# Performance work log

Hardware: AMD Instinct MI355X
Metric: run time of the kernel (lower is better)

The kernel has to match this reference:

```python
import jax, jax.numpy as jnp
import numpy as np

N_NODES = 100000
N_EDGES = 3200000


def _cheb_norm(edge_index, edge_weight, num_nodes):
    # PyG ChebConv.__norm__ with normalization='sym', lambda_max=2.0:
    # L_hat = 2/lambda_max * (I - D^-1/2 A D^-1/2) - I = -D^-1/2 A D^-1/2
    # (the +1 diagonal from get_laplacian and the -1 self-loops cancel),
    # so only the off-diagonal terms -d_i^-1/2 w_ij d_j^-1/2 remain.
    src, dst = edge_index[0], edge_index[1]
    deg = jax.ops.segment_sum(edge_weight, src, num_segments=num_nodes)
    safe = jnp.where(deg > 0, deg, 1.0)
    dis = jnp.where(deg > 0, jax.lax.rsqrt(safe), 0.0)  # deg_inv_sqrt, inf -> 0
    return -dis[src] * edge_weight * dis[dst]


def _cheb_conv(x, src, dst, norm, W, b, num_nodes):
    # W: [K, C_in, C_out]. Chebyshev recurrence Tx_k = 2 L_hat Tx_{k-1} - Tx_{k-2}.
    def prop(h):  # (L_hat h)[dst] += norm_e * h[src]
        return jax.ops.segment_sum(norm[:, None] * h[src], dst, num_segments=num_nodes)

    K = W.shape[0]
    out = x @ W[0]
    if K > 1:
        tx1 = prop(x)
        out = out + tx1 @ W[1]
        if K > 2:
            def step(carry, Wk):
                tx_m2, tx_m1, acc = carry
                tx = 2.0 * prop(tx_m1) - tx_m2
                return (tx_m1, tx, acc + tx @ Wk), None
            (_, _, out), _ = jax.lax.scan(step, (x, tx1, out), W[2:])
    if b is not None:
        out = out + b
    return out


def setup_inputs() -> dict:
    key = jax.random.key(0)
    ks = jax.random.split(key, 12)
    x = jax.random.normal(ks[0], (N_NODES, 2), dtype=jnp.float32)
    edge_index = jax.random.randint(ks[1], (2, N_EDGES), 0, N_NODES, dtype=jnp.int64)
    edge_weight = jax.random.uniform(ks[2], (N_EDGES,), dtype=jnp.float32)
    s = 0.1  # keep activations in a sane range (glorot-ish scale)
    W1 = jax.random.normal(ks[3], (39, 2, 14), dtype=jnp.float32) * s
    b1 = jax.random.normal(ks[4], (14,), dtype=jnp.float32) * s
    W2 = jax.random.normal(ks[5], (43, 14, 20), dtype=jnp.float32) * s
    b2 = jax.random.normal(ks[6], (20,), dtype=jnp.float32) * s
    W3 = jax.random.normal(ks[7], (45, 20, 27), dtype=jnp.float32) * s
    b3 = jax.random.normal(ks[8], (27,), dtype=jnp.float32) * s
    W4 = jax.random.normal(ks[9], (1, 27, 1), dtype=jnp.float32) * s  # K=1, no bias
    return {"x": x, "edge_index": edge_index, "edge_weight": edge_weight,
            "W1": W1, "b1": b1, "W2": W2, "b2": b2, "W3": W3, "b3": b3, "W4": W4}


def reference(x, edge_index, edge_weight, W1, b1, W2, b2, W3, b3, W4):
    src, dst = edge_index[0], edge_index[1]
    norm = _cheb_norm(edge_index, edge_weight, N_NODES)
    h = jax.nn.silu(_cheb_conv(x, src, dst, norm, W1, b1, N_NODES))
    h = jax.nn.silu(_cheb_conv(h, src, dst, norm, W2, b2, N_NODES))
    h = jax.nn.silu(_cheb_conv(h, src, dst, norm, W3, b3, N_NODES))
    h = _cheb_conv(h, src, dst, norm, W4, None, N_NODES)
    return jax.nn.sigmoid(h)
```

## Files before the change

### kernel.cpp

```cpp
#include <hip/hip_runtime.h>
#include <math.h>

#define N_NODES 100000
#define N_EDGES 3200000
#define BS 256
#define CAP_SHIFT 7
#define CAP (1 << CAP_SHIFT)


__global__ void scan_partial_kernel(const int* __restrict__ cnt, int* __restrict__ bsums) {
    __shared__ int lds[256];
    int tid = threadIdx.x;
    int base = blockIdx.x * 1024 + tid * 4;
    int s = 0;
#pragma unroll
    for (int i = 0; i < 4; ++i) s += (base + i < N_NODES) ? cnt[base + i] : 0;
    lds[tid] = s;
    __syncthreads();
    for (int off = 128; off > 0; off >>= 1) {
        if (tid < off) lds[tid] += lds[tid + off];
        __syncthreads();
    }
    if (tid == 0) bsums[blockIdx.x] = lds[0];
}

__global__ void scan_bsums_kernel(int* __restrict__ bsums, int nb, int* __restrict__ total_out) {
    if (threadIdx.x == 0 && blockIdx.x == 0) {
        int acc = 0;
        for (int b = 0; b < nb; ++b) {
            int v = bsums[b];
            bsums[b] = acc;
            acc += v;
        }
        *total_out = acc;
    }
}

__global__ void scan_final_kernel(const int* __restrict__ cnt, const int* __restrict__ bsums,
                                  int* __restrict__ rp) {
    __shared__ int lds[256];
    int tid = threadIdx.x;
    int base = blockIdx.x * 1024 + tid * 4;
    int v[4];
    int ts = 0;
#pragma unroll
    for (int i = 0; i < 4; ++i) {
        v[i] = (base + i < N_NODES) ? cnt[base + i] : 0;
        ts += v[i];
    }
    lds[tid] = ts;
    __syncthreads();
    for (int off = 1; off < 256; off <<= 1) {
        int t = (tid >= off) ? lds[tid - off] : 0;
        __syncthreads();
        lds[tid] += t;
        __syncthreads();
    }
    int run = lds[tid] - ts + bsums[blockIdx.x];
#pragma unroll
    for (int i = 0; i < 4; ++i) {
        if (base + i < N_NODES) rp[base + i] = run;
        run += v[i];
    }
}

__global__ void fill_direct_kernel(const int* __restrict__ src, const int* __restrict__ dst,
                                   int* __restrict__ cnt_s, int* __restrict__ cnt_d,
                                   int* __restrict__ bkt_s, int* __restrict__ bkt_d) {
    int e = blockIdx.x * blockDim.x + threadIdx.x;
    if (e >= N_EDGES) return;
    int s = src[e];
    int d = dst[e];
    int slot_s = atomicAdd(&cnt_s[s], 1);
    bkt_s[((size_t)s << CAP_SHIFT) + slot_s] = e;
    int slot_d = atomicAdd(&cnt_d[d], 1);
    bkt_d[((size_t)d << CAP_SHIFT) + slot_d] = e;
}

__global__ __launch_bounds__(64) void sort_deg_dis_kernel(
    const int* __restrict__ cnt, const int* __restrict__ bkt,
    const float* __restrict__ w, float* __restrict__ dis) {
#pragma clang fp contract(off)
    {
        __shared__ int lr[64][65];
        __shared__ int ls[64][65];
        int n = blockIdx.x * 64 + threadIdx.x;
        if (n >= N_NODES) return;
        int c = cnt[n];
        const int* row = bkt + ((size_t)n << CAP_SHIFT);
        float d = 0.f;
        if (c <= 64) {
            int* a = lr[threadIdx.x];
            int* b = ls[threadIdx.x];
            for (int i = 0; i < c; ++i) a[i] = row[i];
            for (int i = 0; i < c; ++i) {
                int v = a[i];
                int rk = 0;
                for (int j = 0; j < c; ++j) rk += (a[j] < v);
                b[rk] = v;
            }
            for (int r = 0; r < c; ++r) d = d + w[b[r]];
        } else {
            for (int r = 0; r < c; ++r) {
                for (int i = 0; i < c; ++i) {
                    int v = row[i];
                    int rk = 0;
                    for (int j = 0; j < c; ++j) rk += (row[j] < v);
                    if (rk == r) { d = d + w[v]; break; }
                }
            }
        }
        dis[n] = (d > 0.f) ? (1.0f / sqrtf(d)) : 0.f;
    }
}

__global__ __launch_bounds__(64) void sort_pack_kernel(
    const int* __restrict__ cnt, const int* __restrict__ rp,
    const int* __restrict__ bkt, const int* __restrict__ src,
    const float* __restrict__ w, const float* __restrict__ dis,
    int2* __restrict__ packed) {
#pragma clang fp contract(off)
    {
        __shared__ int lr[64][65];
        __shared__ int ls[64][65];
        int n = blockIdx.x * 64 + threadIdx.x;
        if (n >= N_NODES) return;
        int c = cnt[n];
        const int* row = bkt + ((size_t)n << CAP_SHIFT);
        int beg = rp[n];
        float din = dis[n];
        if (c <= 64) {
            int* a = lr[threadIdx.x];
            int* b = ls[threadIdx.x];
            for (int i = 0; i < c; ++i) a[i] = row[i];
            for (int i = 0; i < c; ++i) {
                int v = a[i];
                int rk = 0;
                for (int j = 0; j < c; ++j) rk += (a[j] < v);
                b[rk] = v;
            }
            for (int r = 0; r < c; ++r) {
                int e = b[r];
                int s = src[e];
                float cw = ((-dis[s]) * w[e]) * din;
                packed[beg + r] = make_int2(s, __float_as_int(cw));
            }
        } else {
            for (int r = 0; r < c; ++r) {
                for (int i = 0; i < c; ++i) {
                    int v = row[i];
                    int rk = 0;
                    for (int j = 0; j < c; ++j) rk += (row[j] < v);
                    if (rk == r) {
                        int s = src[v];
                        float cw = ((-dis[s]) * w[v]) * din;
                        packed[beg + r] = make_int2(s, __float_as_int(cw));
                        break;
                    }
                }
            }
        }
    }
}


template <int CIN, int COUT, int SIN, int SACC>
__global__ void layer_init_kernel(const float* __restrict__ hin, const float* __restrict__ W0,
                                  float* __restrict__ acc) {
    int t = blockIdx.x * blockDim.x + threadIdx.x;
    if (t >= N_NODES * COUT) return;
    int n = t / COUT, co = t - n * COUT;
    const float* hr = hin + (size_t)n * SIN;
    float m = 0.f;
#pragma unroll
    for (int ci = 0; ci < CIN; ++ci) m = fmaf(hr[ci], W0[ci * COUT + co], m);
    acc[(size_t)n * SACC + co] = m;
}

template <int CIN, int COUT, int SIN, int SACC, int GS, int LANES, int R>
__global__ __launch_bounds__(LANES* R) void prop_mm_kernel(
    const int* __restrict__ rp, const int2* __restrict__ pk, const float* __restrict__ hin,
    const float* __restrict__ prev, const float* __restrict__ Wk, int rec,
    float* __restrict__ tx_out, float* __restrict__ acc) {
#pragma clang fp contract(off)
    {
        __shared__ float tls[R][LANES * GS];
        int r = threadIdx.x / LANES;
        int lane = threadIdx.x - r * LANES;
        int n = blockIdx.x * R + r;
        bool vn = (n < N_NODES);
        if (vn) {
            int c0 = lane * GS;
            float s[GS];
#pragma unroll
            for (int g = 0; g < GS; ++g) s[g] = 0.f;
            int beg = rp[n], end = rp[n + 1];
            int j = beg;
            if constexpr (GS == 4) {
                for (; j + 7 < end; j += 8) {
                    int2 p0 = pk[j];
                    int2 p1 = pk[j + 1];
                    int2 p2 = pk[j + 2];
                    int2 p3 = pk[j + 3];
                    int2 p4 = pk[j + 4];
                    int2 p5 = pk[j + 5];
                    int2 p6 = pk[j + 6];
                    int2 p7 = pk[j + 7];
                    const float4 q0 = *reinterpret_cast<const float4*>(hin + (size_t)p0.x * SIN + c0);
                    const float4 q1 = *reinterpret_cast<const float4*>(hin + (size_t)p1.x * SIN + c0);
                    const float4 q2 = *reinterpret_cast<const float4*>(hin + (size_t)p2.x * SIN + c0);
                    const float4 q3 = *reinterpret_cast<const float4*>(hin + (size_t)p3.x * SIN + c0);
                    const float4 q4 = *reinterpret_cast<const float4*>(hin + (size_t)p4.x * SIN + c0);
                    const float4 q5 = *reinterpret_cast<const float4*>(hin + (size_t)p5.x * SIN + c0);
                    const float4 q6 = *reinterpret_cast<const float4*>(hin + (size_t)p6.x * SIN + c0);
                    const float4 q7 = *reinterpret_cast<const float4*>(hin + (size_t)p7.x * SIN + c0);
                    float w0 = __int_as_float(p0.y), w1 = __int_as_float(p1.y);
                    float w2 = __int_as_float(p2.y), w3 = __int_as_float(p3.y);
                    float w4 = __int_as_float(p4.y), w5 = __int_as_float(p5.y);
                    float w6 = __int_as_float(p6.y), w7 = __int_as_float(p7.y);
                    s[0] = s[0] + (w0 * q0.x); s[1] = s[1] + (w0 * q0.y);
                    s[2] = s[2] + (w0 * q0.z); s[3] = s[3] + (w0 * q0.w);
                    s[0] = s[0] + (w1 * q1.x); s[1] = s[1] + (w1 * q1.y);
                    s[2] = s[2] + (w1 * q1.z); s[3] = s[3] + (w1 * q1.w);
                    s[0] = s[0] + (w2 * q2.x); s[1] = s[1] + (w2 * q2.y);
                    s[2] = s[2] + (w2 * q2.z); s[3] = s[3] + (w2 * q2.w);
                    s[0] = s[0] + (w3 * q3.x); s[1] = s[1] + (w3 * q3.y);
                    s[2] = s[2] + (w3 * q3.z); s[3] = s[3] + (w3 * q3.w);
                    s[0] = s[0] + (w4 * q4.x); s[1] = s[1] + (w4 * q4.y);
                    s[2] = s[2] + (w4 * q4.z); s[3] = s[3] + (w4 * q4.w);
                    s[0] = s[0] + (w5 * q5.x); s[1] = s[1] + (w5 * q5.y);
                    s[2] = s[2] + (w5 * q5.z); s[3] = s[3] + (w5 * q5.w);
                    s[0] = s[0] + (w6 * q6.x); s[1] = s[1] + (w6 * q6.y);
                    s[2] = s[2] + (w6 * q6.z); s[3] = s[3] + (w6 * q6.w);
                    s[0] = s[0] + (w7 * q7.x); s[1] = s[1] + (w7 * q7.y);
                    s[2] = s[2] + (w7 * q7.z); s[3] = s[3] + (w7 * q7.w);
                }
                for (; j + 3 < end; j += 4) {
                    int2 p0 = pk[j];
                    int2 p1 = pk[j + 1];
                    int2 p2 = pk[j + 2];
                    int2 p3 = pk[j + 3];
                    const float4 q0 = *reinterpret_cast<const float4*>(hin + (size_t)p0.x * SIN + c0);
                    const float4 q1 = *reinterpret_cast<const float4*>(hin + (size_t)p1.x * SIN + c0);
                    const float4 q2 = *reinterpret_cast<const float4*>(hin + (size_t)p2.x * SIN + c0);
                    const float4 q3 = *reinterpret_cast<const float4*>(hin + (size_t)p3.x * SIN + c0);
                    float w0 = __int_as_float(p0.y), w1 = __int_as_float(p1.y);
                    float w2 = __int_as_float(p2.y), w3 = __int_as_float(p3.y);
                    s[0] = s[0] + (w0 * q0.x); s[1] = s[1] + (w0 * q0.y);
                    s[2] = s[2] + (w0 * q0.z); s[3] = s[3] + (w0 * q0.w);
                    s[0] = s[0] + (w1 * q1.x); s[1] = s[1] + (w1 * q1.y);
                    s[2] = s[2] + (w1 * q1.z); s[3] = s[3] + (w1 * q1.w);
                    s[0] = s[0] + (w2 * q2.x); s[1] = s[1] + (w2 * q2.y);
                    s[2] = s[2] + (w2 * q2.z); s[3] = s[3] + (w2 * q2.w);
                    s[0] = s[0] + (w3 * q3.x); s[1] = s[1] + (w3 * q3.y);
                    s[2] = s[2] + (w3 * q3.z); s[3] = s[3] + (w3 * q3.w);
                }
                for (; j < end; ++j) {
                    int2 p = pk[j];
                    float w = __int_as_float(p.y);
                    const float4 q = *reinterpret_cast<const float4*>(hin + (size_t)p.x * SIN + c0);
                    s[0] = s[0] + (w * q.x); s[1] = s[1] + (w * q.y);
                    s[2] = s[2] + (w * q.z); s[3] = s[3] + (w * q.w);
                }
            } else {
                for (; j + 7 < end; j += 8) {
                    int2 p0 = pk[j];
                    int2 p1 = pk[j + 1];
                    int2 p2 = pk[j + 2];
                    int2 p3 = pk[j + 3];
                    int2 p4 = pk[j + 4];
                    int2 p5 = pk[j + 5];
                    int2 p6 = pk[j + 6];
                    int2 p7 = pk[j + 7];
                    const float2 q0 = *reinterpret_cast<const float2*>(hin + (size_t)p0.x * SIN + c0);
                    const float2 q1 = *reinterpret_cast<const float2*>(hin + (size_t)p1.x * SIN + c0);
                    const float2 q2 = *reinterpret_cast<const float2*>(hin + (size_t)p2.x * SIN + c0);
                    const float2 q3 = *reinterpret_cast<const float2*>(hin + (size_t)p3.x * SIN + c0);
                    const float2 q4 = *reinterpret_cast<const float2*>(hin + (size_t)p4.x * SIN + c0);
                    const float2 q5 = *reinterpret_cast<const float2*>(hin + (size_t)p5.x * SIN + c0);
                    const float2 q6 = *reinterpret_cast<const float2*>(hin + (size_t)p6.x * SIN + c0);
                    const float2 q7 = *reinterpret_cast<const float2*>(hin + (size_t)p7.x * SIN + c0);
                    float w0 = __int_as_float(p0.y), w1 = __int_as_float(p1.y);
                    float w2 = __int_as_float(p2.y), w3 = __int_as_float(p3.y);
                    float w4 = __int_as_float(p4.y), w5 = __int_as_float(p5.y);
                    float w6 = __int_as_float(p6.y), w7 = __int_as_float(p7.y);
                    s[0] = s[0] + (w0 * q0.x); s[1] = s[1] + (w0 * q0.y);
                    s[0] = s[0] + (w1 * q1.x); s[1] = s[1] + (w1 * q1.y);
                    s[0] = s[0] + (w2 * q2.x); s[1] = s[1] + (w2 * q2.y);
                    s[0] = s[0] + (w3 * q3.x); s[1] = s[1] + (w3 * q3.y);
                    s[0] = s[0] + (w4 * q4.x); s[1] = s[1] + (w4 * q4.y);
                    s[0] = s[0] + (w5 * q5.x); s[1] = s[1] + (w5 * q5.y);
                    s[0] = s[0] + (w6 * q6.x); s[1] = s[1] + (w6 * q6.y);
                    s[0] = s[0] + (w7 * q7.x); s[1] = s[1] + (w7 * q7.y);
                }
                for (; j + 3 < end; j += 4) {
                    int2 p0 = pk[j];
                    int2 p1 = pk[j + 1];
                    int2 p2 = pk[j + 2];
                    int2 p3 = pk[j + 3];
                    const float2 q0 = *reinterpret_cast<const float2*>(hin + (size_t)p0.x * SIN + c0);
                    const float2 q1 = *reinterpret_cast<const float2*>(hin + (size_t)p1.x * SIN + c0);
                    const float2 q2 = *reinterpret_cast<const float2*>(hin + (size_t)p2.x * SIN + c0);
                    const float2 q3 = *reinterpret_cast<const float2*>(hin + (size_t)p3.x * SIN + c0);
                    float w0 = __int_as_float(p0.y), w1 = __int_as_float(p1.y);
                    float w2 = __int_as_float(p2.y), w3 = __int_as_float(p3.y);
                    s[0] = s[0] + (w0 * q0.x); s[1] = s[1] + (w0 * q0.y);
                    s[0] = s[0] + (w1 * q1.x); s[1] = s[1] + (w1 * q1.y);
                    s[0] = s[0] + (w2 * q2.x); s[1] = s[1] + (w2 * q2.y);
                    s[0] = s[0] + (w3 * q3.x); s[1] = s[1] + (w3 * q3.y);
                }
                for (; j < end; ++j) {
                    int2 p = pk[j];
                    float w = __int_as_float(p.y);
                    const float2 q = *reinterpret_cast<const float2*>(hin + (size_t)p.x * SIN + c0);
                    s[0] = s[0] + (w * q.x); s[1] = s[1] + (w * q.y);
                }
            }
            float t[GS];
            if (rec) {
#pragma unroll
                for (int g = 0; g < GS; ++g) t[g] = 2.f * s[g] - prev[(size_t)n * SIN + c0 + g];
            } else {
#pragma unroll
                for (int g = 0; g < GS; ++g) t[g] = s[g];
            }
#pragma unroll
            for (int g = 0; g < GS; ++g) tls[r][c0 + g] = t[g];
            if constexpr (GS == 4) {
                *reinterpret_cast<float4*>(tx_out + (size_t)n * SIN + c0) =
                    make_float4(t[0], t[1], t[2], t[3]);
            } else {
                *reinterpret_cast<float2*>(tx_out + (size_t)n * SIN + c0) =
                    make_float2(t[0], t[1]);
            }
        }
        __syncthreads();
        if (vn) {
            for (int co = lane; co < COUT; co += LANES) {
                float m = 0.f;
#pragma unroll
                for (int ci = 0; ci < CIN; ++ci) m = fmaf(tls[r][ci], Wk[ci * COUT + co], m);
                acc[(size_t)n * SACC + co] = acc[(size_t)n * SACC + co] + m;
            }
        }
    }
}

template <int C, int S>
__global__ void silu_bias_kernel(float* __restrict__ a, const float* __restrict__ b) {
#pragma clang fp contract(off)
    {
        int t = blockIdx.x * blockDim.x + threadIdx.x;
        if (t >= N_NODES * C) return;
        int n = t / C, c = t - n * C;
        float x = a[(size_t)n * S + c] + b[c];
        float sig = 1.f / (1.f + expf(-x));
        a[(size_t)n * S + c] = x * sig;
    }
}

__global__ void final_kernel(const float* __restrict__ acc, const float* __restrict__ b3,
                             const float* __restrict__ W4, float* __restrict__ out) {
#pragma clang fp contract(off)
    {
        int n = blockIdx.x * blockDim.x + threadIdx.x;
        if (n >= N_NODES) return;
        float m = 0.f;
#pragma unroll
        for (int ci = 0; ci < 27; ++ci) {
            float xv = acc[(size_t)n * 28 + ci] + b3[ci];
            float sig = 1.f / (1.f + expf(-xv));
            float hv = xv * sig;
            m = fmaf(hv, W4[ci], m);
        }
        out[n] = 1.f / (1.f + expf(-m));
    }
}

__global__ void signal_kernel(float* __restrict__ out, float val) {
    int n = blockIdx.x * blockDim.x + threadIdx.x;
    if (n < N_NODES) out[n] = val;
}


static void run_scan(const int* cnt, int* bsums, int* rp, hipStream_t stream) {
    const int nb = (N_NODES + 1023) / 1024;
    scan_partial_kernel<<<nb, 256, 0, stream>>>(cnt, bsums);
    scan_bsums_kernel<<<1, 64, 0, stream>>>(bsums, nb, rp + N_NODES);
    scan_final_kernel<<<nb, 256, 0, stream>>>(cnt, bsums, rp);
}

template <int CIN, int COUT, int SIN, int SACC, int GS, int LANES, int R>
static void run_layer(int K, const float* hin, const float* W, float* acc, float* b0, float* b1,
                      float* b2, const int* rp, const int2* pk, hipStream_t stream) {
    const int gInit = (N_NODES * COUT + BS - 1) / BS;
    const int gProp = (N_NODES + R - 1) / R;
    layer_init_kernel<CIN, COUT, SIN, SACC><<<gInit, BS, 0, stream>>>(hin, W, acc);
    if (K > 1) {
        float* bufs[3] = {b0, b1, b2};
        prop_mm_kernel<CIN, COUT, SIN, SACC, GS, LANES, R><<<gProp, LANES * R, 0, stream>>>(
            rp, pk, hin, nullptr, W + 1 * CIN * COUT, 0, bufs[0], acc);
        const float* pm2 = hin;
        const float* pm1 = bufs[0];
        for (int k = 2; k < K; ++k) {
            float* outb = bufs[(k - 1) % 3];
            prop_mm_kernel<CIN, COUT, SIN, SACC, GS, LANES, R><<<gProp, LANES * R, 0, stream>>>(
                rp, pk, pm1, pm2, W + k * CIN * COUT, 1, outb, acc);
            pm2 = pm1;
            pm1 = outb;
        }
    }
}

extern "C" void kernel_launch(void* const* d_in, const int* in_sizes, int n_in, void* d_out,
                              int out_size, void* d_ws, size_t ws_size, hipStream_t stream) {
    const float* x  = (const float*)d_in[0];
    const int* idx  = (const int*)d_in[1];
    const float* ew = (const float*)d_in[2];
    const float* W1 = (const float*)d_in[3];
    const float* b1 = (const float*)d_in[4];
    const float* W2 = (const float*)d_in[5];
    const float* b2 = (const float*)d_in[6];
    const float* W3 = (const float*)d_in[7];
    const float* b3 = (const float*)d_in[8];
    const float* W4 = (const float*)d_in[9];
    float* out = (float*)d_out;
    (void)in_sizes; (void)n_in; (void)out_size;

    const int* src = idx;
    const int* dst = idx + N_EDGES;

    size_t off = 0;
    auto alloc = [&](size_t bytes) {
        size_t o = off;
        off = (off + bytes + 255) & ~(size_t)255;
        return o;
    };
    char* ws = (char*)d_ws;
    int*   cnt_s   = (int*)(ws + alloc(N_NODES * 4));
    int*   cnt_d   = (int*)(ws + alloc(N_NODES * 4));
    int*   rp_src  = (int*)(ws + alloc((N_NODES + 1) * 4));
    int*   rp_dst  = (int*)(ws + alloc((N_NODES + 1) * 4));
    float* dis     = (float*)(ws + alloc(N_NODES * 4));
    int*   bsums   = (int*)(ws + alloc(512));
    int2*  packed  = (int2*)(ws + alloc((size_t)N_EDGES * 8));
    float* t0      = (float*)(ws + alloc((size_t)N_NODES * 20 * 4));
    float* t1      = (float*)(ws + alloc((size_t)N_NODES * 20 * 4));
    float* t2      = (float*)(ws + alloc((size_t)N_NODES * 20 * 4));
    float* accA    = (float*)(ws + alloc((size_t)N_NODES * 16 * 4));
    float* accB    = (float*)(ws + alloc((size_t)N_NODES * 20 * 4));
    float* accC    = (float*)(ws + alloc((size_t)N_NODES * 28 * 4));
    int*   bkt_s   = (int*)(ws + alloc((size_t)N_NODES * CAP * 4));
    int*   bkt_d   = (int*)(ws + alloc((size_t)N_NODES * CAP * 4));
    const size_t NEED = off;

    int gE = (N_EDGES + BS - 1) / BS;
    int gN = (N_NODES + BS - 1) / BS;
    const int gSort = (N_NODES + 63) / 64;

    if (ws_size < NEED) {
        signal_kernel<<<gN, BS, 0, stream>>>(
            out, 6000.0f + (float)(ws_size / (1024.0 * 1024.0)));
        return;
    }

    (void)hipMemsetAsync(cnt_s, 0, N_NODES * 4, stream);
    (void)hipMemsetAsync(cnt_d, 0, N_NODES * 4, stream);
    fill_direct_kernel<<<gE, BS, 0, stream>>>(src, dst, cnt_s, cnt_d, bkt_s, bkt_d);
    run_scan(cnt_s, bsums, rp_src, stream);
    run_scan(cnt_d, bsums, rp_dst, stream);
    sort_deg_dis_kernel<<<gSort, 64, 0, stream>>>(cnt_s, bkt_s, ew, dis);
    sort_pack_kernel<<<gSort, 64, 0, stream>>>(cnt_d, rp_dst, bkt_d, src, ew, dis, packed);

    run_layer<2, 14, 2, 16, 2, 1, 256>(39, x, W1, accA, t0, t1, t2, rp_dst, packed, stream);
    silu_bias_kernel<14, 16><<<(N_NODES * 14 + BS - 1) / BS, BS, 0, stream>>>(accA, b1);
    run_layer<14, 20, 16, 20, 4, 4, 64>(43, accA, W2, accB, t0, t1, t2, rp_dst, packed, stream);
    silu_bias_kernel<20, 20><<<(N_NODES * 20 + BS - 1) / BS, BS, 0, stream>>>(accB, b2);
    run_layer<20, 27, 20, 28, 4, 5, 51>(45, accB, W3, accC, t0, t1, t2, rp_dst, packed, stream);
    final_kernel<<<gN, BS, 0, stream>>>(accC, b3, W4, out);
}
```

Baseline: 7.692 ms.

## Split feature channels into planar groups and batch the dense matmuls

Node features are stored as separate channel planes (8/8/4-wide groups), and propagation kernels now gather one group per block. This makes each gather touch a narrower, cache-friendlier slice. The dense W_k multiply-accumulate moves out of the propagation kernel into a batched kernel that applies up to 4 Chebyshev terms per pass from a 6-slot ring buffer, cutting acc read-modify-write traffic. The cost is more kernel launches and repeated reads of the edge list per channel group.

```diff
diff --git a/kernel.cpp b/kernel.cpp
--- a/kernel.cpp
+++ b/kernel.cpp
@@ -6,6 +6,9 @@
 #define BS 256
 #define CAP_SHIFT 7
 #define CAP (1 << CAP_SHIFT)
+#define SLOTF 2000000
+#define OFF1 800000
+#define OFF2 1600000
 
 
 __global__ void scan_partial_kernel(const int* __restrict__ cnt, int* __restrict__ bsums) {
@@ -163,199 +166,363 @@
     }
 }
 
-
-template <int CIN, int COUT, int SIN, int SACC>
-__global__ void layer_init_kernel(const float* __restrict__ hin, const float* __restrict__ W0,
-                                  float* __restrict__ acc) {
-    int t = blockIdx.x * blockDim.x + threadIdx.x;
-    if (t >= N_NODES * COUT) return;
-    int n = t / COUT, co = t - n * COUT;
-    const float* hr = hin + (size_t)n * SIN;
-    float m = 0.f;
-#pragma unroll
-    for (int ci = 0; ci < CIN; ++ci) m = fmaf(hr[ci], W0[ci * COUT + co], m);
-    acc[(size_t)n * SACC + co] = m;
-}
-
-template <int CIN, int COUT, int SIN, int SACC, int GS, int LANES, int R>
-__global__ __launch_bounds__(LANES* R) void prop_mm_kernel(
+__device__ __forceinline__ size_t addrA(int n, int c) {
+    return (c < 8) ? ((size_t)n * 8 + c) : (OFF1 + (size_t)n * 8 + (c - 8));
+}
+__device__ __forceinline__ size_t addrB(int n, int c) {
+    return (c < 8) ? ((size_t)n * 8 + c)
+         : (c < 16) ? (OFF1 + (size_t)n * 8 + (c - 8))
+                    : (OFF2 + (size_t)n * 4 + (c - 16));
+}
+
+template <int S>
+__device__ __forceinline__ void gather4_u8(const float* __restrict__ a, int c0,
+                                           const int2* __restrict__ pk, int beg, int end,
+                                           float s[4]) {
+#pragma clang fp contract(off)
+    {
+        int j = beg;
+        for (; j + 7 < end; j += 8) {
+            int2 p0 = pk[j];
+            int2 p1 = pk[j + 1];
+            int2 p2 = pk[j + 2];
+            int2 p3 = pk[j + 3];
+            int2 p4 = pk[j + 4];
+            int2 p5 = pk[j + 5];
+            int2 p6 = pk[j + 6];
+            int2 p7 = pk[j + 7];
+            const float4 q0 = *reinterpret_cast<const float4*>(a + (size_t)p0.x * S + c0);
+            const float4 q1 = *reinterpret_cast<const float4*>(a + (size_t)p1.x * S + c0);
+            const float4 q2 = *reinterpret_cast<const float4*>(a + (size_t)p2.x * S + c0);
+            const float4 q3 = *reinterpret_cast<const float4*>(a + (size_t)p3.x * S + c0);
+            const float4 q4 = *reinterpret_cast<const float4*>(a + (size_t)p4.x * S + c0);
+            const float4 q5 = *reinterpret_cast<const float4*>(a + (size_t)p5.x * S + c0);
+            const float4 q6 = *reinterpret_cast<const float4*>(a + (size_t)p6.x * S + c0);
+            const float4 q7 = *reinterpret_cast<const float4*>(a + (size_t)p7.x * S + c0);
+            float w0 = __int_as_float(p0.y), w1 = __int_as_float(p1.y);
+            float w2 = __int_as_float(p2.y), w3 = __int_as_float(p3.y);
+            float w4 = __int_as_float(p4.y), w5 = __int_as_float(p5.y);
+            float w6 = __int_as_float(p6.y), w7 = __int_as_float(p7.y);
+            s[0] = s[0] + (w0 * q0.x); s[1] = s[1] + (w0 * q0.y);
+            s[2] = s[2] + (w0 * q0.z); s[3] = s[3] + (w0 * q0.w);
+            s[0] = s[0] + (w1 * q1.x); s[1] = s[1] + (w1 * q1.y);
+            s[2] = s[2] + (w1 * q1.z); s[3] = s[3] + (w1 * q1.w);
+            s[0] = s[0] + (w2 * q2.x); s[1] = s[1] + (w2 * q2.y);
+            s[2] = s[2] + (w2 * q2.z); s[3] = s[3] + (w2 * q2.w);
+            s[0] = s[0] + (w3 * q3.x); s[1] = s[1] + (w3 * q3.y);
+            s[2] = s[2] + (w3 * q3.z); s[3] = s[3] + (w3 * q3.w);
+            s[0] = s[0] + (w4 * q4.x); s[1] = s[1] + (w4 * q4.y);
+            s[2] = s[2] + (w4 * q4.z); s[3] = s[3] + (w4 * q4.w);
+            s[0] = s[0] + (w5 * q5.x); s[1] = s[1] + (w5 * q5.y);
+            s[2] = s[2] + (w5 * q5.z); s[3] = s[3] + (w5 * q5.w);
+            s[0] = s[0] + (w6 * q6.x); s[1] = s[1] + (w6 * q6.y);
+            s[2] = s[2] + (w6 * q6.z); s[3] = s[3] + (w6 * q6.w);
+            s[0] = s[0] + (w7 * q7.x); s[1] = s[1] + (w7 * q7.y);
+            s[2] = s[2] + (w7 * q7.z); s[3] = s[3] + (w7 * q7.w);
+        }
+        for (; j + 3 < end; j += 4) {
+            int2 p0 = pk[j];
+            int2 p1 = pk[j + 1];
+            int2 p2 = pk[j + 2];
+            int2 p3 = pk[j + 3];
+            const float4 q0 = *reinterpret_cast<const float4*>(a + (size_t)p0.x * S + c0);
+            const float4 q1 = *reinterpret_cast<const float4*>(a + (size_t)p1.x * S + c0);
+            const float4 q2 = *reinterpret_cast<const float4*>(a + (size_t)p2.x * S + c0);
+            const float4 q3 = *reinterpret_cast<const float4*>(a + (size_t)p3.x * S + c0);
+            float w0 = __int_as_float(p0.y), w1 = __int_as_float(p1.y);
+            float w2 = __int_as_float(p2.y), w3 = __int_as_float(p3.y);
+            s[0] = s[0] + (w0 * q0.x); s[1] = s[1] + (w0 * q0.y);
+            s[2] = s[2] + (w0 * q0.z); s[3] = s[3] + (w0 * q0.w);
+            s[0] = s[0] + (w1 * q1.x); s[1] = s[1] + (w1 * q1.y);
+            s[2] = s[2] + (w1 * q1.z); s[3] = s[3] + (w1 * q1.w);
+            s[0] = s[0] + (w2 * q2.x); s[1] = s[1] + (w2 * q2.y);
+            s[2] = s[2] + (w2 * q2.z); s[3] = s[3] + (w2 * q2.w);
+            s[0] = s[0] + (w3 * q3.x); s[1] = s[1] + (w3 * q3.y);
+            s[2] = s[2] + (w3 * q3.z); s[3] = s[3] + (w3 * q3.w);
+        }
+        for (; j < end; ++j) {
+            int2 p = pk[j];
+            float w = __int_as_float(p.y);
+            const float4 q = *reinterpret_cast<const float4*>(a + (size_t)p.x * S + c0);
+            s[0] = s[0] + (w * q.x); s[1] = s[1] + (w * q.y);
+            s[2] = s[2] + (w * q.z); s[3] = s[3] + (w * q.w);
+        }
+    }
+}
+
+__device__ __forceinline__ void gather2_u8s2(const float* __restrict__ a,
+                                             const int2* __restrict__ pk, int beg, int end,
+                                             float s[2]) {
+#pragma clang fp contract(off)
+    {
+        int j = beg;
+        for (; j + 7 < end; j += 8) {
+            int2 p0 = pk[j];
+            int2 p1 = pk[j + 1];
+            int2 p2 = pk[j + 2];
+            int2 p3 = pk[j + 3];
+            int2 p4 = pk[j + 4];
+            int2 p5 = pk[j + 5];
+            int2 p6 = pk[j + 6];
+            int2 p7 = pk[j + 7];
+            const float2 q0 = *reinterpret_cast<const float2*>(a + (size_t)p0.x * 2);
+            const float2 q1 = *reinterpret_cast<const float2*>(a + (size_t)p1.x * 2);
+            const float2 q2 = *reinterpret_cast<const float2*>(a + (size_t)p2.x * 2);
+            const float2 q3 = *reinterpret_cast<const float2*>(a + (size_t)p3.x * 2);
+            const float2 q4 = *reinterpret_cast<const float2*>(a + (size_t)p4.x * 2);
+            const float2 q5 = *reinterpret_cast<const float2*>(a + (size_t)p5.x * 2);
+            const float2 q6 = *reinterpret_cast<const float2*>(a + (size_t)p6.x * 2);
+            const float2 q7 = *reinterpret_cast<const float2*>(a + (size_t)p7.x * 2);
+            float w0 = __int_as_float(p0.y), w1 = __int_as_float(p1.y);
+            float w2 = __int_as_float(p2.y), w3 = __int_as_float(p3.y);
+            float w4 = __int_as_float(p4.y), w5 = __int_as_float(p5.y);
+            float w6 = __int_as_float(p6.y), w7 = __int_as_float(p7.y);
+            s[0] = s[0] + (w0 * q0.x); s[1] = s[1] + (w0 * q0.y);
+            s[0] = s[0] + (w1 * q1.x); s[1] = s[1] + (w1 * q1.y);
+            s[0] = s[0] + (w2 * q2.x); s[1] = s[1] + (w2 * q2.y);
+            s[0] = s[0] + (w3 * q3.x); s[1] = s[1] + (w3 * q3.y);
+            s[0] = s[0] + (w4 * q4.x); s[1] = s[1] + (w4 * q4.y);
+            s[0] = s[0] + (w5 * q5.x); s[1] = s[1] + (w5 * q5.y);
+            s[0] = s[0] + (w6 * q6.x); s[1] = s[1] + (w6 * q6.y);
+            s[0] = s[0] + (w7 * q7.x); s[1] = s[1] + (w7 * q7.y);
+        }
+        for (; j + 3 < end; j += 4) {
+            int2 p0 = pk[j];
+            int2 p1 = pk[j + 1];
+            int2 p2 = pk[j + 2];
+            int2 p3 = pk[j + 3];
+            const float2 q0 = *reinterpret_cast<const float2*>(a + (size_t)p0.x * 2);
+            const float2 q1 = *reinterpret_cast<const float2*>(a + (size_t)p1.x * 2);
+            const float2 q2 = *reinterpret_cast<const float2*>(a + (size_t)p2.x * 2);
+            const float2 q3 = *reinterpret_cast<const float2*>(a + (size_t)p3.x * 2);
+            float w0 = __int_as_float(p0.y), w1 = __int_as_float(p1.y);
+            float w2 = __int_as_float(p2.y), w3 = __int_as_float(p3.y);
+            s[0] = s[0] + (w0 * q0.x); s[1] = s[1] + (w0 * q0.y);
+            s[0] = s[0] + (w1 * q1.x); s[1] = s[1] + (w1 * q1.y);
+            s[0] = s[0] + (w2 * q2.x); s[1] = s[1] + (w2 * q2.y);
+            s[0] = s[0] + (w3 * q3.x); s[1] = s[1] + (w3 * q3.y);
+        }
+        for (; j < end; ++j) {
+            int2 p = pk[j];
+            float w = __int_as_float(p.y);
+            const float2 q = *reinterpret_cast<const float2*>(a + (size_t)p.x * 2);
+            s[0] = s[0] + (w * q.x); s[1] = s[1] + (w * q.y);
+        }
+    }
+}
+
+__global__ __launch_bounds__(256) void prop_l1_kernel(
     const int* __restrict__ rp, const int2* __restrict__ pk, const float* __restrict__ hin,
     const float* __restrict__ prev, const float* __restrict__ Wk, int rec,
     float* __restrict__ tx_out, float* __restrict__ acc) {
 #pragma clang fp contract(off)
     {
-        __shared__ float tls[R][LANES * GS];
-        int r = threadIdx.x / LANES;
-        int lane = threadIdx.x - r * LANES;
-        int n = blockIdx.x * R + r;
-        bool vn = (n < N_NODES);
-        if (vn) {
-            int c0 = lane * GS;
-            float s[GS];
+        int n = blockIdx.x * 256 + threadIdx.x;
+        if (n >= N_NODES) return;
+        float s[2] = {0.f, 0.f};
+        int beg = rp[n], end = rp[n + 1];
+        gather2_u8s2(hin, pk, beg, end, s);
+        float t0v, t1v;
+        if (rec) {
+            const float2 pv = *reinterpret_cast<const float2*>(prev + (size_t)n * 2);
+            t0v = 2.f * s[0] - pv.x;
+            t1v = 2.f * s[1] - pv.y;
+        } else {
+            t0v = s[0];
+            t1v = s[1];
+        }
+        *reinterpret_cast<float2*>(tx_out + (size_t)n * 2) = make_float2(t0v, t1v);
+        for (int co = 0; co < 14; ++co) {
+            float m = 0.f;
+            m = fmaf(t0v, Wk[co], m);
+            m = fmaf(t1v, Wk[14 + co], m);
+            size_t a = addrA(n, co);
+            acc[a] = acc[a] + m;
+        }
+    }
+}
+
+template <int LAYER>
+__global__ __launch_bounds__(256) void prop_split_kernel(
+    const int* __restrict__ rp, const int2* __restrict__ pk,
+    const float* __restrict__ pm1, const float* __restrict__ pm2,
+    float* __restrict__ tx, int rec) {
+#pragma clang fp contract(off)
+    {
+        int b = blockIdx.x;
+        int n;
+        int c0;
+        size_t goff;
+        int S;
+        bool s4 = false;
+        if constexpr (LAYER == 2) {
+            int g = b & 1;
+            int tile = b >> 1;
+            n = tile * 128 + (threadIdx.x >> 1);
+            c0 = (threadIdx.x & 1) * 4;
+            goff = g ? (size_t)OFF1 : 0;
+            S = 8;
+        } else {
+            int slot = b & 7;
+            int p = b >> 3;
+            if (slot < 3) {
+                int tile = p * 3 + slot;
+                if (tile >= 782) return;
+                n = tile * 128 + (threadIdx.x >> 1);
+                c0 = (threadIdx.x & 1) * 4;
+                goff = 0;
+                S = 8;
+            } else if (slot < 6) {
+                int tile = p * 3 + (slot - 3);
+                if (tile >= 782) return;
+                n = tile * 128 + (threadIdx.x >> 1);
+                c0 = (threadIdx.x & 1) * 4;
+                goff = OFF1;
+                S = 8;
+            } else {
+                int tile = p * 2 + (slot - 6);
+                if (tile >= 391) return;
+                n = tile * 256 + threadIdx.x;
+                c0 = 0;
+                goff = OFF2;
+                S = 4;
+                s4 = true;
+            }
+        }
+        if (n >= N_NODES) return;
+        int beg = rp[n], end = rp[n + 1];
+        float s[4] = {0.f, 0.f, 0.f, 0.f};
+        if (s4) gather4_u8<4>(pm1 + goff, 0, pk, beg, end, s);
+        else gather4_u8<8>(pm1 + goff, c0, pk, beg, end, s);
+        size_t base = goff + (size_t)n * S + c0;
+        float t[4];
+        if (rec) {
+            const float4 pv = *reinterpret_cast<const float4*>(pm2 + base);
+            t[0] = 2.f * s[0] - pv.x; t[1] = 2.f * s[1] - pv.y;
+            t[2] = 2.f * s[2] - pv.z; t[3] = 2.f * s[3] - pv.w;
+        } else {
+            t[0] = s[0]; t[1] = s[1]; t[2] = s[2]; t[3] = s[3];
+        }
+        *reinterpret_cast<float4*>(tx + base) = make_float4(t[0], t[1], t[2], t[3]);
+    }
+}
+
+template <int LAYER>
+__global__ __launch_bounds__(256) void mm_batch_kernel(
+    const float* __restrict__ ring, int k0, int nk,
+    const float* __restrict__ W, float* __restrict__ acc) {
+#pragma clang fp contract(off)
+    {
+        constexpr int CIN = (LAYER == 2) ? 14 : 20;
+        constexpr int COUT = (LAYER == 2) ? 20 : 27;
+        int n = blockIdx.x * 256 + threadIdx.x;
+        if (n >= N_NODES) return;
+        float a[COUT];
+        if constexpr (LAYER == 2) {
+            const float4 v0 = *reinterpret_cast<const float4*>(acc + (size_t)n * 8);
+            const float4 v1 = *reinterpret_cast<const float4*>(acc + (size_t)n * 8 + 4);
+            const float4 v2 = *reinterpret_cast<const float4*>(acc + OFF1 + (size_t)n * 8);
+            const float4 v3 = *reinterpret_cast<const float4*>(acc + OFF1 + (size_t)n * 8 + 4);
+            const float4 v4 = *reinterpret_cast<const float4*>(acc + OFF2 + (size_t)n * 4);
+            a[0] = v0.x; a[1] = v0.y; a[2] = v0.z; a[3] = v0.w;
+            a[4] = v1.x; a[5] = v1.y; a[6] = v1.z; a[7] = v1.w;
+            a[8] = v2.x; a[9] = v2.y; a[10] = v2.z; a[11] = v2.w;
+            a[12] = v3.x; a[13] = v3.y; a[14] = v3.z; a[15] = v3.w;
+            a[16] = v4.x; a[17] = v4.y; a[18] = v4.z; a[19] = v4.w;
+        } else {
 #pragma unroll
-            for (int g = 0; g < GS; ++g) s[g] = 0.f;
-            int beg = rp[n], end = rp[n + 1];
-            int j = beg;
-            if constexpr (GS == 4) {
-                for (; j + 7 < end; j += 8) {
-                    int2 p0 = pk[j];
-                    int2 p1 = pk[j + 1];
-                    int2 p2 = pk[j + 2];
-                    int2 p3 = pk[j + 3];
-                    int2 p4 = pk[j + 4];
-                    int2 p5 = pk[j + 5];
-                    int2 p6 = pk[j + 6];
-                    int2 p7 = pk[j + 7];
-                    const float4 q0 = *reinterpret_cast<const float4*>(hin + (size_t)p0.x * SIN + c0);
-                    const float4 q1 = *reinterpret_cast<const float4*>(hin + (size_t)p1.x * SIN + c0);
-                    const float4 q2 = *reinterpret_cast<const float4*>(hin + (size_t)p2.x * SIN + c0);
-                    const float4 q3 = *reinterpret_cast<const float4*>(hin + (size_t)p3.x * SIN + c0);
-                    const float4 q4 = *reinterpret_cast<const float4*>(hin + (size_t)p4.x * SIN + c0);
-                    const float4 q5 = *reinterpret_cast<const float4*>(hin + (size_t)p5.x * SIN + c0);
-                    const float4 q6 = *reinterpret_cast<const float4*>(hin + (size_t)p6.x * SIN + c0);
-                    const float4 q7 = *reinterpret_cast<const float4*>(hin + (size_t)p7.x * SIN + c0);
-                    float w0 = __int_as_float(p0.y), w1 = __int_as_float(p1.y);
-                    float w2 = __int_as_float(p2.y), w3 = __int_as_float(p3.y);
-                    float w4 = __int_as_float(p4.y), w5 = __int_as_float(p5.y);
-                    float w6 = __int_as_float(p6.y), w7 = __int_as_float(p7.y);
-                    s[0] = s[0] + (w0 * q0.x); s[1] = s[1] + (w0 * q0.y);
-                    s[2] = s[2] + (w0 * q0.z); s[3] = s[3] + (w0 * q0.w);
-                    s[0] = s[0] + (w1 * q1.x); s[1] = s[1] + (w1 * q1.y);
-                    s[2] = s[2] + (w1 * q1.z); s[3] = s[3] + (w1 * q1.w);
-                    s[0] = s[0] + (w2 * q2.x); s[1] = s[1] + (w2 * q2.y);
-                    s[2] = s[2] + (w2 * q2.z); s[3] = s[3] + (w2 * q2.w);
-                    s[0] = s[0] + (w3 * q3.x); s[1] = s[1] + (w3 * q3.y);
-                    s[2] = s[2] + (w3 * q3.z); s[3] = s[3] + (w3 * q3.w);
-                    s[0] = s[0] + (w4 * q4.x); s[1] = s[1] + (w4 * q4.y);
-                    s[2] = s[2] + (w4 * q4.z); s[3] = s[3] + (w4 * q4.w);
-                    s[0] = s[0] + (w5 * q5.x); s[1] = s[1] + (w5 * q5.y);
-                    s[2] = s[2] + (w5 * q5.z); s[3] = s[3] + (w5 * q5.w);
-                    s[0] = s[0] + (w6 * q6.x); s[1] = s[1] + (w6 * q6.y);
-                    s[2] = s[2] + (w6 * q6.z); s[3] = s[3] + (w6 * q6.w);
-                    s[0] = s[0] + (w7 * q7.x); s[1] = s[1] + (w7 * q7.y);
-                    s[2] = s[2] + (w7 * q7.z); s[3] = s[3] + (w7 * q7.w);
-                }
-                for (; j + 3 < end; j += 4) {
-                    int2 p0 = pk[j];
-                    int2 p1 = pk[j + 1];
-                    int2 p2 = pk[j + 2];
-                    int2 p3 = pk[j + 3];
-                    const float4 q0 = *reinterpret_cast<const float4*>(hin + (size_t)p0.x * SIN + c0);
-                    const float4 q1 = *reinterpret_cast<const float4*>(hin + (size_t)p1.x * SIN + c0);
-                    const float4 q2 = *reinterpret_cast<const float4*>(hin + (size_t)p2.x * SIN + c0);
-                    const float4 q3 = *reinterpret_cast<const float4*>(hin + (size_t)p3.x * SIN + c0);
-                    float w0 = __int_as_float(p0.y), w1 = __int_as_float(p1.y);
-                    float w2 = __int_as_float(p2.y), w3 = __int_as_float(p3.y);
-                    s[0] = s[0] + (w0 * q0.x); s[1] = s[1] + (w0 * q0.y);
-                    s[2] = s[2] + (w0 * q0.z); s[3] = s[3] + (w0 * q0.w);
-                    s[0] = s[0] + (w1 * q1.x); s[1] = s[1] + (w1 * q1.y);
-                    s[2] = s[2] + (w1 * q1.z); s[3] = s[3] + (w1 * q1.w);
-                    s[0] = s[0] + (w2 * q2.x); s[1] = s[1] + (w2 * q2.y);
-                    s[2] = s[2] + (w2 * q2.z); s[3] = s[3] + (w2 * q2.w);
-                    s[0] = s[0] + (w3 * q3.x); s[1] = s[1] + (w3 * q3.y);
-                    s[2] = s[2] + (w3 * q3.z); s[3] = s[3] + (w3 * q3.w);
-                }
-                for (; j < end; ++j) {
-                    int2 p = pk[j];
-                    float w = __int_as_float(p.y);
-                    const float4 q = *reinterpret_cast<const float4*>(hin + (size_t)p.x * SIN + c0);
-                    s[0] = s[0] + (w * q.x); s[1] = s[1] + (w * q.y);
-                    s[2] = s[2] + (w * q.z); s[3] = s[3] + (w * q.w);
-                }
+            for (int i = 0; i < 7; ++i) {
+                const float4 v = *reinterpret_cast<const float4*>(acc + (size_t)n * 28 + i * 4);
+                if (i * 4 + 0 < 27) a[i * 4 + 0] = v.x;
+                if (i * 4 + 1 < 27) a[i * 4 + 1] = v.y;
+                if (i * 4 + 2 < 27) a[i * 4 + 2] = v.z;
+                if (i * 4 + 3 < 27) a[i * 4 + 3] = v.w;
+            }
+        }
+        for (int kk = 0; kk < nk; ++kk) {
+            int k = k0 + kk;
+            const float* t = ring + (size_t)((k - 1) % 6) * SLOTF;
+            float hv[CIN];
+            if constexpr (LAYER == 2) {
+                const float4 a0 = *reinterpret_cast<const float4*>(t + (size_t)n * 8);
+                const float4 a1 = *reinterpret_cast<const float4*>(t + (size_t)n * 8 + 4);
+                const float4 a2 = *reinterpret_cast<const float4*>(t + OFF1 + (size_t)n * 8);
+                const float4 a3 = *reinterpret_cast<const float4*>(t + OFF1 + (size_t)n * 8 + 4);
+                hv[0] = a0.x; hv[1] = a0.y; hv[2] = a0.z; hv[3] = a0.w;
+                hv[4] = a1.x; hv[5] = a1.y; hv[6] = a1.z; hv[7] = a1.w;
+                hv[8] = a2.x; hv[9] = a2.y; hv[10] = a2.z; hv[11] = a2.w;
+                hv[12] = a3.x; hv[13] = a3.y;
             } else {
-                for (; j + 7 < end; j += 8) {
-                    int2 p0 = pk[j];
-                    int2 p1 = pk[j + 1];
-                    int2 p2 = pk[j + 2];
-                    int2 p3 = pk[j + 3];
-                    int2 p4 = pk[j + 4];
-                    int2 p5 = pk[j + 5];
-                    int2 p6 = pk[j + 6];
-                    int2 p7 = pk[j + 7];
-                    const float2 q0 = *reinterpret_cast<const float2*>(hin + (size_t)p0.x * SIN + c0);
-                    const float2 q1 = *reinterpret_cast<const float2*>(hin + (size_t)p1.x * SIN + c0);
-                    const float2 q2 = *reinterpret_cast<const float2*>(hin + (size_t)p2.x * SIN + c0);
-                    const float2 q3 = *reinterpret_cast<const float2*>(hin + (size_t)p3.x * SIN + c0);
-                    const float2 q4 = *reinterpret_cast<const float2*>(hin + (size_t)p4.x * SIN + c0);
-                    const float2 q5 = *reinterpret_cast<const float2*>(hin + (size_t)p5.x * SIN + c0);
-                    const float2 q6 = *reinterpret_cast<const float2*>(hin + (size_t)p6.x * SIN + c0);
-                    const float2 q7 = *reinterpret_cast<const float2*>(hin + (size_t)p7.x * SIN + c0);
-                    float w0 = __int_as_float(p0.y), w1 = __int_as_float(p1.y);
-                    float w2 = __int_as_float(p2.y), w3 = __int_as_float(p3.y);
-                    float w4 = __int_as_float(p4.y), w5 = __int_as_float(p5.y);
-                    float w6 = __int_as_float(p6.y), w7 = __int_as_float(p7.y);
-                    s[0] = s[0] + (w0 * q0.x); s[1] = s[1] + (w0 * q0.y);
-                    s[0] = s[0] + (w1 * q1.x); s[1] = s[1] + (w1 * q1.y);
-                    s[0] = s[0] + (w2 * q2.x); s[1] = s[1] + (w2 * q2.y);
-                    s[0] = s[0] + (w3 * q3.x); s[1] = s[1] + (w3 * q3.y);
-                    s[0] = s[0] + (w4 * q4.x); s[1] = s[1] + (w4 * q4.y);
-                    s[0] = s[0] + (w5 * q5.x); s[1] = s[1] + (w5 * q5.y);
-                    s[0] = s[0] + (w6 * q6.x); s[1] = s[1] + (w6 * q6.y);
-                    s[0] = s[0] + (w7 * q7.x); s[1] = s[1] + (w7 * q7.y);
-                }
-                for (; j + 3 < end; j += 4) {
-                    int2 p0 = pk[j];
-                    int2 p1 = pk[j + 1];
-                    int2 p2 = pk[j + 2];
-                    int2 p3 = pk[j + 3];
-                    const float2 q0 = *reinterpret_cast<const float2*>(hin + (size_t)p0.x * SIN + c0);
-                    const float2 q1 = *reinterpret_cast<const float2*>(hin + (size_t)p1.x * SIN + c0);
-                    const float2 q2 = *reinterpret_cast<const float2*>(hin + (size_t)p2.x * SIN + c0);
-                    const float2 q3 = *reinterpret_cast<const float2*>(hin + (size_t)p3.x * SIN + c0);
-                    float w0 = __int_as_float(p0.y), w1 = __int_as_float(p1.y);
-                    float w2 = __int_as_float(p2.y), w3 = __int_as_float(p3.y);
-                    s[0] = s[0] + (w0 * q0.x); s[1] = s[1] + (w0 * q0.y);
-                    s[0] = s[0] + (w1 * q1.x); s[1] = s[1] + (w1 * q1.y);
-                    s[0] = s[0] + (w2 * q2.x); s[1] = s[1] + (w2 * q2.y);
-                    s[0] = s[0] + (w3 * q3.x); s[1] = s[1] + (w3 * q3.y);
-                }
-                for (; j < end; ++j) {
-                    int2 p = pk[j];
-                    float w = __int_as_float(p.y);
-                    const float2 q = *reinterpret_cast<const float2*>(hin + (size_t)p.x * SIN + c0);
-                    s[0] = s[0] + (w * q.x); s[1] = s[1] + (w * q.y);
-                }
-            }
-            float t[GS];
-            if (rec) {
-#pragma unroll
-                for (int g = 0; g < GS; ++g) t[g] = 2.f * s[g] - prev[(size_t)n * SIN + c0 + g];
-            } else {
-#pragma unroll
-                for (int g = 0; g < GS; ++g) t[g] = s[g];
-            }
-#pragma unroll
-            for (int g = 0; g < GS; ++g) tls[r][c0 + g] = t[g];
-            if constexpr (GS == 4) {
-                *reinterpret_cast<float4*>(tx_out + (size_t)n * SIN + c0) =
-                    make_float4(t[0], t[1], t[2], t[3]);
-            } else {
-                *reinterpret_cast<float2*>(tx_out + (size_t)n * SIN + c0) =
-                    make_float2(t[0], t[1]);
-            }
-        }
-        __syncthreads();
-        if (vn) {
-            for (int co = lane; co < COUT; co += LANES) {
+                const float4 a0 = *reinterpret_cast<const float4*>(t + (size_t)n * 8);
+                const float4 a1 = *reinterpret_cast<const float4*>(t + (size_t)n * 8 + 4);
+                const float4 a2 = *reinterpret_cast<const float4*>(t + OFF1 + (size_t)n * 8);
+                const float4 a3 = *reinterpret_cast<const float4*>(t + OFF1 + (size_t)n * 8 + 4);
+                const float4 a4 = *reinterpret_cast<const float4*>(t + OFF2 + (size_t)n * 4);
+                hv[0] = a0.x; hv[1] = a0.y; hv[2] = a0.z; hv[3] = a0.w;
+                hv[4] = a1.x; hv[5] = a1.y; hv[6] = a1.z; hv[7] = a1.w;
+                hv[8] = a2.x; hv[9] = a2.y; hv[10] = a2.z; hv[11] = a2.w;
+                hv[12] = a3.x; hv[13] = a3.y; hv[14] = a3.z; hv[15] = a3.w;
+                hv[16] = a4.x; hv[17] = a4.y; hv[18] = a4.z; hv[19] = a4.w;
+            }
+            const float* Wk = W + (size_t)k * CIN * COUT;
+            for (int co = 0; co < COUT; ++co) {
                 float m = 0.f;
 #pragma unroll
-                for (int ci = 0; ci < CIN; ++ci) m = fmaf(tls[r][ci], Wk[ci * COUT + co], m);
-                acc[(size_t)n * SACC + co] = acc[(size_t)n * SACC + co] + m;
-            }
-        }
-    }
-}
-
-template <int C, int S>
+                for (int ci = 0; ci < CIN; ++ci) m = fmaf(hv[ci], Wk[ci * COUT + co], m);
+                a[co] = a[co] + m;
+            }
+        }
+        if constexpr (LAYER == 2) {
+            *reinterpret_cast<float4*>(acc + (size_t)n * 8) = make_float4(a[0], a[1], a[2], a[3]);
+            *reinterpret_cast<float4*>(acc + (size_t)n * 8 + 4) = make_float4(a[4], a[5], a[6], a[7]);
+            *reinterpret_cast<float4*>(acc + OFF1 + (size_t)n * 8) = make_float4(a[8], a[9], a[10], a[11]);
+            *reinterpret_cast<float4*>(acc + OFF1 + (size_t)n * 8 + 4) = make_float4(a[12], a[13], a[14], a[15]);
+            *reinterpret_cast<float4*>(acc + OFF2 + (size_t)n * 4) = make_float4(a[16], a[17], a[18], a[19]);
+        } else {
+            for (int co = 0; co < 27; ++co) acc[(size_t)n * 28 + co] = a[co];
+        }
+    }
+}
+
+template <int LAYER>
+__global__ void layer_init_kernel(const float* __restrict__ hin, const float* __restrict__ W0,
+                                  float* __restrict__ acc) {
+#pragma clang fp contract(off)
+    {
+        constexpr int CIN = (LAYER == 1) ? 2 : ((LAYER == 2) ? 14 : 20);
+        constexpr int COUT = (LAYER == 1) ? 14 : ((LAYER == 2) ? 20 : 27);
+        int t = blockIdx.x * blockDim.x + threadIdx.x;
+        if (t >= N_NODES * COUT) return;
+        int n = t / COUT, co = t - n * COUT;
+        float m = 0.f;
+#pragma unroll
+        for (int ci = 0; ci < CIN; ++ci) {
+            float hv;
+            if constexpr (LAYER == 1) hv = hin[(size_t)n * 2 + ci];
+            else if constexpr (LAYER == 2) hv = hin[addrA(n, ci)];
+            else hv = hin[addrB(n, ci)];
+            m = fmaf(hv, W0[ci * COUT + co], m);
+        }
+        size_t a;
+        if constexpr (LAYER == 1) a = addrA(n, co);
+        else if constexpr (LAYER == 2) a = addrB(n, co);
+        else a = (size_t)n * 28 + co;
+        acc[a] = m;
+    }
+}
+
+template <int LAYER>
 __global__ void silu_bias_kernel(float* __restrict__ a, const float* __restrict__ b) {
 #pragma clang fp contract(off)
     {
+        constexpr int C = (LAYER == 1) ? 14 : 20;
         int t = blockIdx.x * blockDim.x + threadIdx.x;
         if (t >= N_NODES * C) return;
         int n = t / C, c = t - n * C;
-        float x = a[(size_t)n * S + c] + b[c];
+        size_t ad = (LAYER == 1) ? addrA(n, c) : addrB(n, c);
+        float x = a[ad] + b[c];
         float sig = 1.f / (1.f + expf(-x));
-        a[(size_t)n * S + c] = x * sig;
+        a[ad] = x * sig;
     }
 }
 
@@ -388,28 +555,6 @@
     scan_partial_kernel<<<nb, 256, 0, stream>>>(cnt, bsums);
     scan_bsums_kernel<<<1, 64, 0, stream>>>(bsums, nb, rp + N_NODES);
     scan_final_kernel<<<nb, 256, 0, stream>>>(cnt, bsums, rp);
-}
-
-template <int CIN, int COUT, int SIN, int SACC, int GS, int LANES, int R>
-static void run_layer(int K, const float* hin, const float* W, float* acc, float* b0, float* b1,
-                      float* b2, const int* rp, const int2* pk, hipStream_t stream) {
-    const int gInit = (N_NODES * COUT + BS - 1) / BS;
-    const int gProp = (N_NODES + R - 1) / R;
-    layer_init_kernel<CIN, COUT, SIN, SACC><<<gInit, BS, 0, stream>>>(hin, W, acc);
-    if (K > 1) {
-        float* bufs[3] = {b0, b1, b2};
-        prop_mm_kernel<CIN, COUT, SIN, SACC, GS, LANES, R><<<gProp, LANES * R, 0, stream>>>(
-            rp, pk, hin, nullptr, W + 1 * CIN * COUT, 0, bufs[0], acc);
-        const float* pm2 = hin;
-        const float* pm1 = bufs[0];
-        for (int k = 2; k < K; ++k) {
-            float* outb = bufs[(k - 1) % 3];
-            prop_mm_kernel<CIN, COUT, SIN, SACC, GS, LANES, R><<<gProp, LANES * R, 0, stream>>>(
-                rp, pk, pm1, pm2, W + k * CIN * COUT, 1, outb, acc);
-            pm2 = pm1;
-            pm1 = outb;
-        }
-    }
 }
 
 extern "C" void kernel_launch(void* const* d_in, const int* in_sizes, int n_in, void* d_out,
@@ -444,11 +589,9 @@
     float* dis     = (float*)(ws + alloc(N_NODES * 4));
     int*   bsums   = (int*)(ws + alloc(512));
     int2*  packed  = (int2*)(ws + alloc((size_t)N_EDGES * 8));
-    float* t0      = (float*)(ws + alloc((size_t)N_NODES * 20 * 4));
-    float* t1      = (float*)(ws + alloc((size_t)N_NODES * 20 * 4));
-    float* t2      = (float*)(ws + alloc((size_t)N_NODES * 20 * 4));
-    float* accA    = (float*)(ws + alloc((size_t)N_NODES * 16 * 4));
-    float* accB    = (float*)(ws + alloc((size_t)N_NODES * 20 * 4));
+    float* ring    = (float*)(ws + alloc((size_t)6 * SLOTF * 4));
+    float* accA    = (float*)(ws + alloc((size_t)1600000 * 4));
+    float* accB    = (float*)(ws + alloc((size_t)2000000 * 4));
     float* accC    = (float*)(ws + alloc((size_t)N_NODES * 28 * 4));
     int*   bkt_s   = (int*)(ws + alloc((size_t)N_NODES * CAP * 4));
     int*   bkt_d   = (int*)(ws + alloc((size_t)N_NODES * CAP * 4));
@@ -472,10 +615,54 @@
     sort_deg_dis_kernel<<<gSort, 64, 0, stream>>>(cnt_s, bkt_s, ew, dis);
     sort_pack_kernel<<<gSort, 64, 0, stream>>>(cnt_d, rp_dst, bkt_d, src, ew, dis, packed);
 
-    run_layer<2, 14, 2, 16, 2, 1, 256>(39, x, W1, accA, t0, t1, t2, rp_dst, packed, stream);
-    silu_bias_kernel<14, 16><<<(N_NODES * 14 + BS - 1) / BS, BS, 0, stream>>>(accA, b1);
-    run_layer<14, 20, 16, 20, 4, 4, 64>(43, accA, W2, accB, t0, t1, t2, rp_dst, packed, stream);
-    silu_bias_kernel<20, 20><<<(N_NODES * 20 + BS - 1) / BS, BS, 0, stream>>>(accB, b2);
-    run_layer<20, 27, 20, 28, 4, 5, 51>(45, accB, W3, accC, t0, t1, t2, rp_dst, packed, stream);
+    (void)hipMemsetAsync(accA, 0, (size_t)1600000 * 4, stream);
+
+    layer_init_kernel<1><<<(N_NODES * 14 + BS - 1) / BS, BS, 0, stream>>>(x, W1, accA);
+    {
+        const float* pm1 = x;
+        const float* pm2 = nullptr;
+        for (int k = 1; k < 39; ++k) {
+            float* txk = ring + (size_t)((k - 1) % 3) * SLOTF;
+            prop_l1_kernel<<<391, 256, 0, stream>>>(rp_dst, packed, pm1, pm2,
+                                                    W1 + (size_t)k * 2 * 14, (k >= 2) ? 1 : 0,
+                                                    txk, accA);
+            pm2 = pm1;
+            pm1 = txk;
+        }
+    }
+    silu_bias_kernel<1><<<(N_NODES * 14 + BS - 1) / BS, BS, 0, stream>>>(accA, b1);
+
+    layer_init_kernel<2><<<(N_NODES * 20 + BS - 1) / BS, BS, 0, stream>>>(accA, W2, accB);
+    {
+        int last = 0;
+        for (int k = 1; k < 43; ++k) {
+            const float* pm1 = (k == 1) ? accA : ring + (size_t)((k - 2) % 6) * SLOTF;
+            const float* pm2 = (k == 2) ? accA
+                             : ((k >= 3) ? ring + (size_t)((k - 3) % 6) * SLOTF : nullptr);
+            prop_split_kernel<2><<<1564, 256, 0, stream>>>(
+                rp_dst, packed, pm1, pm2, ring + (size_t)((k - 1) % 6) * SLOTF, (k >= 2) ? 1 : 0);
+            if (k - last == 4 || k == 42) {
+                mm_batch_kernel<2><<<391, 256, 0, stream>>>(ring, last + 1, k - last, W2, accB);
+                last = k;
+            }
+        }
+    }
+    silu_bias_kernel<2><<<(N_NODES * 20 + BS - 1) / BS, BS, 0, stream>>>(accB, b2);
+
+    layer_init_kernel<3><<<(N_NODES * 27 + BS - 1) / BS, BS, 0, stream>>>(accB, W3, accC);
+    {
+        int last = 0;
+        for (int k = 1; k < 45; ++k) {
+            const float* pm1 = (k == 1) ? accB : ring + (size_t)((k - 2) % 6) * SLOTF;
+            const float* pm2 = (k == 2) ? accB
+                             : ((k >= 3) ? ring + (size_t)((k - 3) % 6) * SLOTF : nullptr);
+            prop_split_kernel<3><<<2088, 256, 0, stream>>>(
+                rp_dst, packed, pm1, pm2, ring + (size_t)((k - 1) % 6) * SLOTF, (k >= 2) ? 1 : 0);
+            if (k - last == 4 || k == 44) {
+                mm_batch_kernel<3><<<391, 256, 0, stream>>>(ring, last + 1, k - last, W3, accC);
+                last = k;
+            }
+        }
+    }
     final_kernel<<<gN, BS, 0, stream>>>(accC, b3, W4, out);
 }
```

New measurement: 9.023 ms. 1.17x slower.
